# Kernel optimization log

Hardware: AMD Instinct MI355X
Metric: run time of the kernel (lower is better)

## Reference

```python
import math
import jax
import jax.numpy as jnp
import numpy as np

NUM_TOKENS = 8192
MODEL_DIM = 2048
NUM_EXPERTS = 64
CAPACITY_FACTOR = 1.0


def setup_inputs() -> dict:
    key = jax.random.key(0)
    k1, k2 = jax.random.split(key)
    x = jax.random.normal(k1, (NUM_TOKENS, MODEL_DIM), dtype=jnp.float32)
    # gate weight, torch Linear layout [num_experts, model_dim]
    wg = jax.random.normal(k2, (NUM_EXPERTS, MODEL_DIM), dtype=jnp.float32) / np.sqrt(MODEL_DIM).astype(np.float32)
    return {"x": x, "wg": wg}


def top2gating(logits, capacity_factor):
    s, e = logits.shape  # static under jit
    capacity = int(math.ceil(2 * s / e * capacity_factor))
    gates = jax.nn.softmax(logits, axis=1)  # [s, e]

    # top-1 expert
    indices1_s = jnp.argmax(gates, axis=1)
    mask1 = jax.nn.one_hot(indices1_s, e, dtype=jnp.int32)  # [s, e]

    # top-2 expert via gumbel-perturbed logits with expert-1 masked out
    gumbel = jax.random.gumbel(jax.random.key(42), logits.shape, dtype=logits.dtype)
    logits_w_noise = logits + gumbel
    logits_except1 = jnp.where(mask1.astype(bool), -jnp.inf, logits_w_noise)
    indices2_s = jnp.argmax(logits_except1, axis=1)
    mask2 = jax.nn.one_hot(indices2_s, e, dtype=jnp.int32)

    # positions within each expert's buffer (prefix sums over tokens)
    locations1 = jnp.cumsum(mask1, axis=0) - 1  # [s, e]
    locations2 = jnp.cumsum(mask2, axis=0) - 1
    locations2 = locations2 + jnp.sum(mask1, axis=0, keepdims=True)

    # load-balancing aux loss
    me = jnp.mean(gates, axis=0)
    ce = jnp.mean(mask1.astype(gates.dtype), axis=0)
    l_aux = jnp.mean(me * ce) * (e * e)

    # drop tokens beyond capacity
    mask1 = mask1 * (locations1 < capacity).astype(jnp.int32)
    mask2 = mask2 * (locations2 < capacity).astype(jnp.int32)

    locations1_s = jnp.sum(locations1 * mask1, axis=1)  # [s]
    locations2_s = jnp.sum(locations2 * mask2, axis=1)

    mask1_f = mask1.astype(gates.dtype)
    mask2_f = mask2.astype(gates.dtype)
    gates1_s = jnp.sum(gates * mask1_f, axis=1)  # [s]
    gates2_s = jnp.sum(gates * mask2_f, axis=1)
    denom_s = jnp.maximum(gates1_s + gates2_s, jnp.finfo(gates.dtype).eps)
    gates1_s = gates1_s / denom_s
    gates2_s = gates2_s / denom_s

    gates1 = gates1_s[:, None] * mask1_f  # [s, e]
    gates2 = gates2_s[:, None] * mask2_f

    locations1_sc = jax.nn.one_hot(locations1_s, capacity, dtype=gates.dtype)  # [s, c]
    locations2_sc = jax.nn.one_hot(locations2_s, capacity, dtype=gates.dtype)

    combine_weights = (gates1[:, :, None] * locations1_sc[:, None, :]
                       + gates2[:, :, None] * locations2_sc[:, None, :])  # [s, e, c]
    dispatch_mask = combine_weights.astype(bool)
    return l_aux, combine_weights, dispatch_mask


def reference(x, wg):
    logits = x @ wg.T  # [s, e]
    return top2gating(logits, CAPACITY_FACTOR)
```

## Files before the change

kernel.cpp:

```cpp
#include <hip/hip_runtime.h>
#include <hip/hip_bf16.h>
#include <stdint.h>

#define TOKENS 8192
#define DIM 2048
#define EXPERTS 64
#define CAP 256
#define COMB_ELEMS ((size_t)TOKENS * EXPERTS * CAP)
#define OUT_ELEMS (1 + 2 * COMB_ELEMS)

#define GEMM_BLOCKS 256
#define ZERO_BLOCKS 2048

__device__ __forceinline__ void tf_round(uint32_t& a, uint32_t& b, int r) {
  a += b;
  b = (b << r) | (b >> (32 - r));
  b ^= a;
}

__device__ __forceinline__ void threefry2x32(uint32_t k0, uint32_t k1,
                                             uint32_t x0, uint32_t x1,
                                             uint32_t& o0, uint32_t& o1) {
  const uint32_t ks0 = k0, ks1 = k1, ks2 = k0 ^ k1 ^ 0x1BD11BDAu;
  x0 += ks0; x1 += ks1;
  tf_round(x0, x1, 13); tf_round(x0, x1, 15); tf_round(x0, x1, 26); tf_round(x0, x1, 6);
  x0 += ks1; x1 += ks2 + 1u;
  tf_round(x0, x1, 17); tf_round(x0, x1, 29); tf_round(x0, x1, 16); tf_round(x0, x1, 24);
  x0 += ks2; x1 += ks0 + 2u;
  tf_round(x0, x1, 13); tf_round(x0, x1, 15); tf_round(x0, x1, 26); tf_round(x0, x1, 6);
  x0 += ks0; x1 += ks1 + 3u;
  tf_round(x0, x1, 17); tf_round(x0, x1, 29); tf_round(x0, x1, 16); tf_round(x0, x1, 24);
  x0 += ks1; x1 += ks2 + 4u;
  tf_round(x0, x1, 13); tf_round(x0, x1, 15); tf_round(x0, x1, 26); tf_round(x0, x1, 6);
  x0 += ks2; x1 += ks0 + 5u;
  o0 = x0; o1 = x1;
}

__global__ __launch_bounds__(256) void k_fused(const float* __restrict__ x,
                                               const float* __restrict__ wg,
                                               float* __restrict__ out,
                                               int* __restrict__ e1, int* __restrict__ e2,
                                               float* __restrict__ g1, float* __restrict__ g2,
                                               float* __restrict__ gpart) {
  __shared__ float xs[32][33];
  __shared__ float wt[32][64];
  __shared__ float gpl[4][64];

  const int tid = threadIdx.x;

  if (blockIdx.x >= GEMM_BLOCKS) {
    const size_t n4 = OUT_ELEMS / 4;
    float4* o4 = reinterpret_cast<float4*>(out);
    const int zb = blockIdx.x - GEMM_BLOCKS;
    size_t i = (size_t)zb * 256 + tid;
    const size_t stride = (size_t)ZERO_BLOCKS * 256;
    const float4 z = make_float4(0.f, 0.f, 0.f, 0.f);
    for (; i < n4; i += stride) o4[i] = z;
    if (zb == 0 && tid == 0) out[2 * COMB_ELEMS] = 0.f;
    return;
  }

  const int tok0 = blockIdx.x * 32;
  const int e0 = (tid & 15) * 4;
  const int t0 = (tid >> 4) * 2;

  const int xr = tid >> 3;
  const int xc = (tid & 7) << 2;
  const int wr = tid >> 2;
  const int wc = (tid & 3) << 3;

  const float* xp = x + (size_t)(tok0 + xr) * DIM + xc;
  const float* wp = wg + (size_t)wr * DIM + wc;

  float4 xv  = *reinterpret_cast<const float4*>(xp);
  float4 wv0 = *reinterpret_cast<const float4*>(wp);
  float4 wv1 = *reinterpret_cast<const float4*>(wp + 4);

  float acc[2][4] = {{0.f, 0.f, 0.f, 0.f}, {0.f, 0.f, 0.f, 0.f}};

  for (int k0 = 0; k0 < DIM; k0 += 32) {
    *reinterpret_cast<float4*>(&xs[xr][xc]) = xv;
    wt[wc + 0][wr] = wv0.x; wt[wc + 1][wr] = wv0.y;
    wt[wc + 2][wr] = wv0.z; wt[wc + 3][wr] = wv0.w;
    wt[wc + 4][wr] = wv1.x; wt[wc + 5][wr] = wv1.y;
    wt[wc + 6][wr] = wv1.z; wt[wc + 7][wr] = wv1.w;
    __syncthreads();
    if (k0 + 32 < DIM) {
      xv  = *reinterpret_cast<const float4*>(xp + k0 + 32);
      wv0 = *reinterpret_cast<const float4*>(wp + k0 + 32);
      wv1 = *reinterpret_cast<const float4*>(wp + k0 + 36);
    }
#pragma unroll
    for (int kk = 0; kk < 32; ++kk) {
      const float4 b = *reinterpret_cast<const float4*>(&wt[kk][e0]);
      const float a0 = xs[t0][kk];
      const float a1 = xs[t0 + 1][kk];
      acc[0][0] = fmaf(a0, b.x, acc[0][0]);
      acc[0][1] = fmaf(a0, b.y, acc[0][1]);
      acc[0][2] = fmaf(a0, b.z, acc[0][2]);
      acc[0][3] = fmaf(a0, b.w, acc[0][3]);
      acc[1][0] = fmaf(a1, b.x, acc[1][0]);
      acc[1][1] = fmaf(a1, b.y, acc[1][1]);
      acc[1][2] = fmaf(a1, b.z, acc[1][2]);
      acc[1][3] = fmaf(a1, b.w, acc[1][3]);
    }
    __syncthreads();
  }

#pragma unroll
  for (int i = 0; i < 2; ++i)
    *reinterpret_cast<float4*>(&wt[t0 + i][e0]) =
        make_float4(acc[i][0], acc[i][1], acc[i][2], acc[i][3]);
  __syncthreads();

  const int w = tid >> 6;
  const int lane = tid & 63;
  float colsum = 0.f;
  for (int lt = w * 8; lt < w * 8 + 8; ++lt) {
    const int t = tok0 + lt;
    const float logit = wt[lt][lane];

    float m = logit;
#pragma unroll
    for (int off = 32; off > 0; off >>= 1) m = fmaxf(m, __shfl_xor(m, off));
    const float ex = expf(logit - m);
    float s = ex;
#pragma unroll
    for (int off = 32; off > 0; off >>= 1) s += __shfl_xor(s, off);
    const float gate = ex / s;
    colsum += gate;

    float v1 = logit; int i1 = lane;
#pragma unroll
    for (int off = 32; off > 0; off >>= 1) {
      const float ov = __shfl_xor(v1, off);
      const int oi = __shfl_xor(i1, off);
      if (ov > v1 || (ov == v1 && oi < i1)) { v1 = ov; i1 = oi; }
    }

    const uint32_t i_flat = (uint32_t)t * 64u + (uint32_t)lane;
    uint32_t b0, b1;
    threefry2x32(0u, 42u, 0u, i_flat, b0, b1);
    const uint32_t bits = b0 ^ b1;
    float u = __uint_as_float((bits >> 9) | 0x3f800000u) - 1.0f;
    u += 1.17549435e-38f;
    const float gum = -logf(-logf(u));
    const float noisy = (lane == i1) ? -__builtin_inff() : (logit + gum);

    float v2 = noisy; int i2 = lane;
#pragma unroll
    for (int off = 32; off > 0; off >>= 1) {
      const float ov = __shfl_xor(v2, off);
      const int oi = __shfl_xor(i2, off);
      if (ov > v2 || (ov == v2 && oi < i2)) { v2 = ov; i2 = oi; }
    }

    const float gate1 = __shfl(gate, i1);
    const float gate2 = __shfl(gate, i2);
    if (lane == 0) { e1[t] = i1; e2[t] = i2; g1[t] = gate1; g2[t] = gate2; }
  }
  gpl[w][lane] = colsum;
  __syncthreads();
  if (w == 0)
    gpart[(size_t)blockIdx.x * 64 + lane] =
        (gpl[0][lane] + gpl[1][lane]) + (gpl[2][lane] + gpl[3][lane]);
}

__global__ __launch_bounds__(256) void k_scan(const int* __restrict__ e1,
    const int* __restrict__ e2, const float* __restrict__ gpart,
    int* __restrict__ loc1, int* __restrict__ loc2,
    int* __restrict__ counts1, float* __restrict__ gsum) {
  const int e = blockIdx.x;
  const int tid = threadIdx.x;
  const int lane = tid & 63;
  const int w = tid >> 6;
  __shared__ int wt4[4];
  __shared__ int carry;
  __shared__ float gw[4];
  if (tid == 0) carry = 0;

  float gp = gpart[(size_t)tid * 64 + e];
#pragma unroll
  for (int off = 32; off > 0; off >>= 1) gp += __shfl_xor(gp, off);
  if (lane == 0) gw[w] = gp;
  __syncthreads();
  if (tid == 0) gsum[e] = (gw[0] + gw[1]) + (gw[2] + gw[3]);

  for (int base = 0; base < TOKENS; base += 256) {
    const int t = base + tid;
    const int p = (e1[t] == e) ? 1 : 0;
    const uint64_t mask = __ballot(p);
    const int rk = __popcll(mask & ((1ull << lane) - 1ull));
    if (lane == 0) wt4[w] = __popcll(mask);
    __syncthreads();
    int pre = carry;
#pragma unroll
    for (int i = 0; i < 4; ++i)
      if (i < w) pre += wt4[i];
    if (p) loc1[t] = pre + rk;
    const int tot = wt4[0] + wt4[1] + wt4[2] + wt4[3];
    __syncthreads();
    if (tid == 0) carry += tot;
  }
  __syncthreads();
  if (tid == 0) counts1[e] = carry;
  for (int base = 0; base < TOKENS; base += 256) {
    const int t = base + tid;
    const int p = (e2[t] == e) ? 1 : 0;
    const uint64_t mask = __ballot(p);
    const int rk = __popcll(mask & ((1ull << lane) - 1ull));
    if (lane == 0) wt4[w] = __popcll(mask);
    __syncthreads();
    int pre = carry;
#pragma unroll
    for (int i = 0; i < 4; ++i)
      if (i < w) pre += wt4[i];
    if (p) loc2[t] = pre + rk;
    const int tot = wt4[0] + wt4[1] + wt4[2] + wt4[3];
    __syncthreads();
    if (tid == 0) carry += tot;
  }
}

__global__ __launch_bounds__(256) void k_scatter(const int* __restrict__ e1,
    const int* __restrict__ e2, const float* __restrict__ g1,
    const float* __restrict__ g2, const int* __restrict__ loc1,
    const int* __restrict__ loc2, const float* __restrict__ gsum,
    const int* __restrict__ counts1, float* __restrict__ out) {
  const int tid = threadIdx.x;
  if (blockIdx.x == 0 && tid < 64) {
    float v = gsum[tid] * (float)counts1[tid];
#pragma unroll
    for (int off = 32; off > 0; off >>= 1) v += __shfl_xor(v, off);
    if (tid == 0) out[0] = v * (1.0f / 1048576.0f);
  }
  const int t = blockIdx.x * 256 + tid;
  const int a = e1[t], b = e2[t];
  const int l1 = loc1[t], l2 = loc2[t];
  const bool k1 = l1 < CAP;
  const bool k2 = l2 < CAP;
  const float ga = k1 ? g1[t] : 0.f;
  const float gb = k2 ? g2[t] : 0.f;
  const float denom = fmaxf(ga + gb, 1.1920929e-07f);
  float* __restrict__ combine = out + 1;
  float* __restrict__ dispatch = out + 1 + COMB_ELEMS;
  if (k1) {
    const size_t idx = ((size_t)t * EXPERTS + a) * CAP + l1;
    combine[idx] = ga / denom;
    dispatch[idx] = 1.0f;
  }
  if (k2) {
    const size_t idx = ((size_t)t * EXPERTS + b) * CAP + l2;
    combine[idx] = gb / denom;
    dispatch[idx] = 1.0f;
  }
}

extern "C" void kernel_launch(void* const* d_in, const int* in_sizes, int n_in,
                              void* d_out, int out_size, void* d_ws, size_t ws_size,
                              hipStream_t stream) {
  const float* x = (const float*)d_in[0];
  const float* wg = (const float*)d_in[1];
  float* out = (float*)d_out;

  int*   e1      = (int*)d_ws;
  int*   e2      = e1 + TOKENS;
  int*   loc1    = e2 + TOKENS;
  int*   loc2    = loc1 + TOKENS;
  int*   counts1 = loc2 + TOKENS;
  float* g1      = (float*)(counts1 + 64);
  float* g2      = g1 + TOKENS;
  float* gsum    = g2 + TOKENS;
  float* gpart   = gsum + 64;

  k_fused<<<GEMM_BLOCKS + ZERO_BLOCKS, 256, 0, stream>>>(x, wg, out, e1, e2, g1, g2, gpart);
  k_scan<<<EXPERTS, 256, 0, stream>>>(e1, e2, gpart, loc1, loc2, counts1, gsum);
  k_scatter<<<TOKENS / 256, 256, 0, stream>>>(e1, e2, g1, g2, loc1, loc2, gsum, counts1, out);
}
```

Measured before the change: 1.143 ms.

## Parallelize expert prefix scan and use nontemporal stores for zero fill

New measurement: 1.144 ms. Within noise of the previous version (+0.2%).

```diff
diff --git a/kernel.cpp b/kernel.cpp
--- a/kernel.cpp
+++ b/kernel.cpp
@@ -11,6 +11,8 @@
 
 #define GEMM_BLOCKS 256
 #define ZERO_BLOCKS 2048
+
+typedef float f32x4 __attribute__((ext_vector_type(4)));
 
 __device__ __forceinline__ void tf_round(uint32_t& a, uint32_t& b, int r) {
   a += b;
@@ -49,13 +51,17 @@
   const int tid = threadIdx.x;
 
   if (blockIdx.x >= GEMM_BLOCKS) {
-    const size_t n4 = OUT_ELEMS / 4;
-    float4* o4 = reinterpret_cast<float4*>(out);
+    f32x4* o4 = reinterpret_cast<f32x4*>(out);
     const int zb = blockIdx.x - GEMM_BLOCKS;
+    const size_t stride = (size_t)ZERO_BLOCKS * 256;
     size_t i = (size_t)zb * 256 + tid;
-    const size_t stride = (size_t)ZERO_BLOCKS * 256;
-    const float4 z = make_float4(0.f, 0.f, 0.f, 0.f);
-    for (; i < n4; i += stride) o4[i] = z;
+    const f32x4 z = {0.f, 0.f, 0.f, 0.f};
+#pragma unroll 4
+    for (int it = 0; it < 64; ++it) {
+      __builtin_nontemporal_store(z, &o4[i]);
+      __builtin_nontemporal_store(z, &o4[i + stride]);
+      i += 2 * stride;
+    }
     if (zb == 0 && tid == 0) out[2 * COMB_ELEMS] = 0.f;
     return;
   }
@@ -174,51 +180,75 @@
   const int tid = threadIdx.x;
   const int lane = tid & 63;
   const int w = tid >> 6;
-  __shared__ int wt4[4];
-  __shared__ int carry;
+  __shared__ int wt1[32][4], wt2[32][4];
+  __shared__ int pre1[32][4], pre2[32][4];
+  __shared__ int c1tot;
   __shared__ float gw[4];
-  if (tid == 0) carry = 0;
 
   float gp = gpart[(size_t)tid * 64 + e];
 #pragma unroll
   for (int off = 32; off > 0; off >>= 1) gp += __shfl_xor(gp, off);
   if (lane == 0) gw[w] = gp;
+
+  const uint64_t ltm = (lane == 0) ? 0ull : ((~0ull) >> (64 - lane));
+
+  int r1[32], r2[32];
+#pragma unroll
+  for (int s = 0; s < 32; ++s) {
+    const int t = s * 256 + tid;
+    const bool q1 = (e1[t] == e);
+    const bool q2 = (e2[t] == e);
+    const uint64_t m1 = __ballot(q1);
+    const uint64_t m2 = __ballot(q2);
+    r1[s] = q1 ? (int)__popcll(m1 & ltm) + 1 : 0;
+    r2[s] = q2 ? (int)__popcll(m2 & ltm) + 1 : 0;
+    if (lane == 0) { wt1[s][w] = (int)__popcll(m1); wt2[s][w] = (int)__popcll(m2); }
+  }
   __syncthreads();
+
   if (tid == 0) gsum[e] = (gw[0] + gw[1]) + (gw[2] + gw[3]);
 
-  for (int base = 0; base < TOKENS; base += 256) {
-    const int t = base + tid;
-    const int p = (e1[t] == e) ? 1 : 0;
-    const uint64_t mask = __ballot(p);
-    const int rk = __popcll(mask & ((1ull << lane) - 1ull));
-    if (lane == 0) wt4[w] = __popcll(mask);
-    __syncthreads();
-    int pre = carry;
-#pragma unroll
-    for (int i = 0; i < 4; ++i)
-      if (i < w) pre += wt4[i];
-    if (p) loc1[t] = pre + rk;
-    const int tot = wt4[0] + wt4[1] + wt4[2] + wt4[3];
-    __syncthreads();
-    if (tid == 0) carry += tot;
+  if (w == 0) {
+    {
+      int va = wt1[lane >> 2][lane & 3];
+      int vb = wt1[(64 + lane) >> 2][(64 + lane) & 3];
+      int sa = va, sb = vb;
+#pragma unroll
+      for (int d = 1; d < 64; d <<= 1) {
+        const int t1 = __shfl_up(sa, d);
+        const int t2 = __shfl_up(sb, d);
+        if (lane >= d) { sa += t1; sb += t2; }
+      }
+      const int tot_a = __shfl(sa, 63);
+      pre1[lane >> 2][lane & 3] = sa - va;
+      pre1[(64 + lane) >> 2][(64 + lane) & 3] = tot_a + sb - vb;
+      if (lane == 63) c1tot = tot_a + sb;
+    }
+    {
+      int va = wt2[lane >> 2][lane & 3];
+      int vb = wt2[(64 + lane) >> 2][(64 + lane) & 3];
+      int sa = va, sb = vb;
+#pragma unroll
+      for (int d = 1; d < 64; d <<= 1) {
+        const int t1 = __shfl_up(sa, d);
+        const int t2 = __shfl_up(sb, d);
+        if (lane >= d) { sa += t1; sb += t2; }
+      }
+      const int tot_a = __shfl(sa, 63);
+      pre2[lane >> 2][lane & 3] = sa - va;
+      pre2[(64 + lane) >> 2][(64 + lane) & 3] = tot_a + sb - vb;
+    }
   }
   __syncthreads();
-  if (tid == 0) counts1[e] = carry;
-  for (int base = 0; base < TOKENS; base += 256) {
-    const int t = base + tid;
-    const int p = (e2[t] == e) ? 1 : 0;
-    const uint64_t mask = __ballot(p);
-    const int rk = __popcll(mask & ((1ull << lane) - 1ull));
-    if (lane == 0) wt4[w] = __popcll(mask);
-    __syncthreads();
-    int pre = carry;
-#pragma unroll
-    for (int i = 0; i < 4; ++i)
-      if (i < w) pre += wt4[i];
-    if (p) loc2[t] = pre + rk;
-    const int tot = wt4[0] + wt4[1] + wt4[2] + wt4[3];
-    __syncthreads();
-    if (tid == 0) carry += tot;
+
+  const int c1 = c1tot;
+  if (tid == 0) counts1[e] = c1;
+
+#pragma unroll
+  for (int s = 0; s < 32; ++s) {
+    const int t = s * 256 + tid;
+    if (r1[s]) loc1[t] = pre1[s][w] + r1[s] - 1;
+    if (r2[s]) loc2[t] = c1 + pre2[s][w] + r2[s] - 1;
   }
 }
 
```
